# Kernel tuning notes

Measured on AMD Instinct MI355X. Metric: run time of the kernel, lower is better.

Reference implementation:

```python
import jax, jax.numpy as jnp
import numpy as np

LOG_2PI = float(np.log(2.0 * np.pi))


def setup_inputs() -> dict:
    key = jax.random.key(0)
    k1, k2, k3 = jax.random.split(key, 3)
    N, D, K = 2_000_000, 16, 32
    data = jax.random.normal(k1, (N, D), dtype=jnp.float32)
    means = jax.random.uniform(k2, (K, D), dtype=jnp.float32)  # torch.rand init
    # torch init is eye expanded per component; perturb slightly so the
    # Cholesky / solve paths are exercised with non-trivial values while
    # A @ A.T stays well-conditioned PD.
    cov_parts = (jnp.eye(D, dtype=jnp.float32)[None, :, :]
                 + 0.1 * jax.random.normal(k3, (K, D, D), dtype=jnp.float32))
    log_weights = jnp.zeros((K,), dtype=jnp.float32)
    return {"data": data, "means": means, "cov_parts": cov_parts,
            "log_weights": log_weights}


def _mixture_loglik(data, means, cov_parts, log_weights):
    D = data.shape[-1]
    # covariance_k = A_k @ A_k^T  -> Cholesky factor L_k (lower)
    cov = jnp.einsum('kij,klj->kil', cov_parts, cov_parts)      # [K, D, D]
    chol = jnp.linalg.cholesky(cov)                             # [K, D, D]

    def comp_logprob(mu, L):
        # MVN log_prob for one component over all N points
        diff = data - mu                                        # [N, D]
        # solve L z = diff^T  -> z: [D, N]
        z = jax.scipy.linalg.solve_triangular(L, diff.T, lower=True)
        quad = jnp.sum(z * z, axis=0)                           # [N]
        logdet = jnp.sum(jnp.log(jnp.diagonal(L)))              # 0.5*logdet(cov)
        return -0.5 * (quad + D * LOG_2PI) - logdet             # [N]

    # [N, K] log-likelihood per point per component
    log_liks = jax.vmap(comp_logprob, in_axes=(0, 0), out_axes=1)(means, chol)
    weighted = log_liks + log_weights ** 2                      # note: squared, per source
    return jnp.mean(jax.nn.logsumexp(weighted, axis=1))


def reference(data, means, cov_parts, log_weights):
    return _mixture_loglik(data, means, cov_parts, log_weights)
```

## Files before the change

### kernel.cpp

```cpp
#include <hip/hip_runtime.h>
#include <math.h>


#define LOG_2PI 1.8378770664093453f
#define INV_LN2 1.4426950408889634f
#define LN2_D   0.6931471805599453

typedef float    float4v __attribute__((ext_vector_type(4)));
typedef float    f32x16  __attribute__((ext_vector_type(16)));
typedef _Float16 f16x8   __attribute__((ext_vector_type(8)));
typedef _Float16 f16x2   __attribute__((ext_vector_type(2)));

union H8 { f16x8 h8; f16x2 h2[4]; };

#if __has_builtin(__builtin_amdgcn_exp2f)
#define EXP2F(x) __builtin_amdgcn_exp2f(x)
#else
#define EXP2F(x) exp2f(x)
#endif
#if __has_builtin(__builtin_amdgcn_logf)
#define LOG2F(x) __builtin_amdgcn_logf(x)
#else
#define LOG2F(x) log2f(x)
#endif

static __device__ __forceinline__ f16x2 pk2(float a, float b) {
#if __has_builtin(__builtin_amdgcn_cvt_pkrtz)
  return __builtin_bit_cast(f16x2, __builtin_amdgcn_cvt_pkrtz(a, b));
#else
  f16x2 r; r[0] = (_Float16)a; r[1] = (_Float16)b; return r;
#endif
}

static __device__ __forceinline__ float partner32(float x, bool lo) {
#if __has_builtin(__builtin_amdgcn_permlane32_swap)
  typedef unsigned u32x2 __attribute__((ext_vector_type(2)));
  unsigned u = __builtin_bit_cast(unsigned, x);
  u32x2 r = __builtin_amdgcn_permlane32_swap(u, u, false, false);
  return __builtin_bit_cast(float, lo ? r[1] : r[0]);
#else
  return __shfl_xor(x, 32, 64);
#endif
}

static __device__ __forceinline__ f16x2 sel2(bool c, f16x2 a, f16x2 b) {
  unsigned ua = __builtin_bit_cast(unsigned, a);
  unsigned ub = __builtin_bit_cast(unsigned, b);
  return __builtin_bit_cast(f16x2, c ? ua : ub);
}

__global__ void setup_kernel(const float* __restrict__ means,
                             const float* __restrict__ cov_parts,
                             const float* __restrict__ log_weights,
                             _Float16* __restrict__ W)
{
  const int k = blockIdx.x;
  const int i = threadIdx.x;

  __shared__ float sA[16][17];
  __shared__ float sC[16][17];
  __shared__ float sMu[16];
  __shared__ float sR[16];

  if (i < 16) {
    #pragma unroll
    for (int j = 0; j < 16; ++j) sA[i][j] = cov_parts[(k*16 + i)*16 + j];
    sMu[i] = means[k*16 + i];
  }
  __syncthreads();

  if (i < 16) {
    #pragma unroll
    for (int j = 0; j < 16; ++j) {
      float acc = 0.f;
      #pragma unroll
      for (int l = 0; l < 16; ++l) acc += sA[i][l] * sA[j][l];
      sC[i][j] = acc;
    }
  }
  __syncthreads();

  for (int j = 0; j < 16; ++j) {
    if (i == j) {
      float d = sC[j][j];
      for (int l = 0; l < j; ++l) d -= sC[j][l]*sC[j][l];
      sC[j][j] = sqrtf(d);
    }
    __syncthreads();
    if (i < 16 && i > j) {
      float a = sC[i][j];
      for (int l = 0; l < j; ++l) a -= sC[i][l]*sC[j][l];
      sC[i][j] = a / sC[j][j];
    }
    __syncthreads();
  }

  if (i < 16) {
    float y[16];
    #pragma unroll
    for (int r = 0; r < 16; ++r) {
      float a = (r == i) ? 1.f : 0.f;
      #pragma unroll
      for (int l = 0; l < r; ++l) a -= sC[r][l] * y[l];
      y[r] = a / sC[r][r];
    }
    #pragma unroll
    for (int r = 0; r < 16; ++r) sA[r][i] = y[r];
  }
  __syncthreads();

  if (i < 16) {
    float p[16];
    #pragma unroll
    for (int j = 0; j < 16; ++j) {
      float acc = 0.f;
      #pragma unroll
      for (int l = 0; l < 16; ++l) acc += sA[l][i] * sA[l][j];
      p[j] = acc;
    }
    float ri = 0.f;
    #pragma unroll
    for (int j = 0; j < 16; ++j) ri += p[j] * sMu[j];
    sR[i] = ri;

    #pragma unroll
    for (int j = 0; j < 16; ++j) {
      W[(size_t)(i*64 + (k + 32*(j >> 3)))*8 + (j & 7)] =
          (_Float16)(-0.5f * INV_LN2 * p[j]);
    }
    W[(size_t)(16*64 + (k + 32*(i >> 3)))*8 + (i & 7)] =
        (_Float16)(INV_LN2 * ri);
  }
  __syncthreads();

  if (i == 0) {
    float logdet = 0.f;
    #pragma unroll
    for (int j = 0; j < 16; ++j) logdet += __logf(sC[j][j]);
    float mupmu = 0.f;
    #pragma unroll
    for (int j = 0; j < 16; ++j) mupmu += sMu[j] * sR[j];
    float lw = log_weights[k];
    float c2v = INV_LN2 * (-0.5f*(mupmu + 16.f*LOG_2PI) - logdet + lw*lw);
    #pragma unroll
    for (int v = 0; v < 8; ++v) {
      W[(size_t)(17*64 + k)*8 + v]      = (v == 0) ? (_Float16)c2v : (_Float16)0.f;
      W[(size_t)(17*64 + k + 32)*8 + v] = (_Float16)0.f;
    }
  }
}

__global__ __launch_bounds__(256, 3) void main_kernel(
    const float* __restrict__ data,
    const _Float16* __restrict__ W,
    float* __restrict__ partials,
    int ntiles)
{
  const int lane = threadIdx.x & 63;
  const int n32  = lane & 31;
  const bool lo  = lane < 32;
  const int gwave  = (int)((blockIdx.x * blockDim.x + threadIdx.x) >> 6);
  const int nwaves = (int)((gridDim.x * blockDim.x) >> 6);

  f16x8 Wf[18];
  #pragma unroll
  for (int c = 0; c < 18; ++c)
    Wf[c] = *(const f16x8*)(W + (size_t)(c*64 + lane)*8);

  H8 bC;
  #pragma unroll
  for (int j = 0; j < 4; ++j) bC.h2[j] = pk2(0.f, 0.f);
  if (lo) bC.h2[0] = pk2(1.f, 0.f);

  float accsum = 0.f;

  const char* ptr = (const char*)data + ((size_t)gwave*2048 + (size_t)n32*64);
  const size_t step = (size_t)nwaves * 2048;

  float4v p0, p1, p2, p3;
  if (gwave < ntiles) {
    p0 = *(const float4v*)(ptr);      p1 = *(const float4v*)(ptr + 16);
    p2 = *(const float4v*)(ptr + 32); p3 = *(const float4v*)(ptr + 48);
  }

  for (int t = gwave; t < ntiles; t += nwaves) {
    f16x2 xh[8];
    xh[0] = pk2(p0[0], p0[1]); xh[1] = pk2(p0[2], p0[3]);
    xh[2] = pk2(p1[0], p1[1]); xh[3] = pk2(p1[2], p1[3]);
    xh[4] = pk2(p2[0], p2[1]); xh[5] = pk2(p2[2], p2[3]);
    xh[6] = pk2(p3[0], p3[1]); xh[7] = pk2(p3[2], p3[3]);

    ptr += step;
    if (t + nwaves < ntiles) {
      p0 = *(const float4v*)(ptr);      p1 = *(const float4v*)(ptr + 16);
      p2 = *(const float4v*)(ptr + 32); p3 = *(const float4v*)(ptr + 48);
    }

    f16x2 xs[4];
    #pragma unroll
    for (int j = 0; j < 4; ++j) xs[j] = sel2(lo, xh[j], xh[4+j]);

    f32x16 acc;
    #pragma unroll
    for (int r = 0; r < 16; ++r) acc[r] = 0.f;

    #pragma unroll
    for (int c = 0; c < 16; ++c) {
      _Float16 xi = xh[c >> 1][c & 1];
      H8 b;
      #pragma unroll
      for (int j = 0; j < 4; ++j) b.h2[j] = xs[j] * xi;
      acc = __builtin_amdgcn_mfma_f32_32x32x16_f16(Wf[c], b.h8, acc, 0, 0, 0);
    }
    {
      H8 b;
      #pragma unroll
      for (int j = 0; j < 4; ++j) b.h2[j] = xs[j];
      acc = __builtin_amdgcn_mfma_f32_32x32x16_f16(Wf[16], b.h8, acc, 0, 0, 0);
    }
    acc = __builtin_amdgcn_mfma_f32_32x32x16_f16(Wf[17], bC.h8, acc, 0, 0, 0);

    float m = acc[0];
    #pragma unroll
    for (int r = 1; r < 16; ++r) m = fmaxf(m, acc[r]);
    m = fmaxf(m, partner32(m, lo));
    float s = 0.f;
    #pragma unroll
    for (int r = 0; r < 16; ++r) s += EXP2F(acc[r] - m);
    s += partner32(s, lo);
    accsum += m + LOG2F(s);
  }

  #pragma unroll
  for (int off = 1; off <= 32; off <<= 1)
    accsum += __shfl_xor(accsum, off, 64);

  __shared__ float wsum[4];
  const int wid = (int)(threadIdx.x >> 6);
  if ((threadIdx.x & 63) == 0) wsum[wid] = accsum;
  __syncthreads();
  if (threadIdx.x == 0)
    partials[blockIdx.x] = wsum[0] + wsum[1] + wsum[2] + wsum[3];
}

__global__ void reduce_kernel(const float* __restrict__ partials, int n,
                              float* __restrict__ out, double scale)
{
  __shared__ double sd[256];
  double a = 0.0;
  for (int idx = threadIdx.x; idx < n; idx += 256) a += (double)partials[idx];
  sd[threadIdx.x] = a;
  __syncthreads();
  for (int s = 128; s > 0; s >>= 1) {
    if ((int)threadIdx.x < s) sd[threadIdx.x] += sd[threadIdx.x + s];
    __syncthreads();
  }
  if (threadIdx.x == 0) out[0] = (float)(sd[0] * scale);
}

extern "C" void kernel_launch(void* const* d_in, const int* in_sizes, int n_in,
                              void* d_out, int out_size, void* d_ws, size_t ws_size,
                              hipStream_t stream)
{
  const float* data        = (const float*)d_in[0];
  const float* means       = (const float*)d_in[1];
  const float* cov_parts   = (const float*)d_in[2];
  const float* log_weights = (const float*)d_in[3];

  const int npts   = in_sizes[0] / 16;
  const int ntiles = npts / 32;

  _Float16* W      = (_Float16*)d_ws;
  float*    partials = (float*)((char*)d_ws + (size_t)18*64*8*sizeof(_Float16));

  const int GRID = 768, BLOCK = 256;
  setup_kernel<<<32, 64, 0, stream>>>(means, cov_parts, log_weights, W);
  main_kernel<<<GRID, BLOCK, 0, stream>>>(data, W, partials, ntiles);
  reduce_kernel<<<1, 256, 0, stream>>>(partials, GRID, (float*)d_out,
                                       LN2_D / (2.0 * (double)npts));
}
```

Baseline: 202.8 us.

## Double-buffer data prefetch and fuse final reduction via last-block atomic counter

The main loop now keeps two tiles in flight, alternating between two register buffers so each load has a full iteration more latency cover. The separate reduce kernel is removed: each block publishes its partial, increments a global counter reset in the setup kernel, and the last block performs the double-precision reduction. This saves one kernel launch and adds prefetch depth, at the cost of extra registers under the occupancy-3 launch bound and an atomic plus fences per block.

```diff
diff --git a/kernel.cpp b/kernel.cpp
--- a/kernel.cpp
+++ b/kernel.cpp
@@ -52,10 +52,13 @@
 __global__ void setup_kernel(const float* __restrict__ means,
                              const float* __restrict__ cov_parts,
                              const float* __restrict__ log_weights,
-                             _Float16* __restrict__ W)
+                             _Float16* __restrict__ W,
+                             unsigned* __restrict__ counter)
 {
   const int k = blockIdx.x;
   const int i = threadIdx.x;
+
+  if (k == 0 && i == 0) counter[0] = 0u;
 
   __shared__ float sA[16][17];
   __shared__ float sC[16][17];
@@ -154,6 +157,9 @@
     const float* __restrict__ data,
     const _Float16* __restrict__ W,
     float* __restrict__ partials,
+    unsigned* __restrict__ counter,
+    float* __restrict__ out,
+    double scale,
     int ntiles)
 {
   const int lane = threadIdx.x & 63;
@@ -174,26 +180,32 @@
 
   float accsum = 0.f;
 
-  const char* ptr = (const char*)data + ((size_t)gwave*2048 + (size_t)n32*64);
-  const size_t step = (size_t)nwaves * 2048;
-
-  float4v p0, p1, p2, p3;
+  const char* ptrA = (const char*)data + ((size_t)gwave*2048 + (size_t)n32*64);
+  const char* ptrB = ptrA + (size_t)nwaves*2048;
+  const size_t step2 = (size_t)nwaves * 4096;
+
+  float4v pA0, pA1, pA2, pA3, pB0, pB1, pB2, pB3;
   if (gwave < ntiles) {
-    p0 = *(const float4v*)(ptr);      p1 = *(const float4v*)(ptr + 16);
-    p2 = *(const float4v*)(ptr + 32); p3 = *(const float4v*)(ptr + 48);
-  }
-
-  for (int t = gwave; t < ntiles; t += nwaves) {
+    pA0 = *(const float4v*)(ptrA);      pA1 = *(const float4v*)(ptrA + 16);
+    pA2 = *(const float4v*)(ptrA + 32); pA3 = *(const float4v*)(ptrA + 48);
+  }
+  if (gwave + nwaves < ntiles) {
+    pB0 = *(const float4v*)(ptrB);      pB1 = *(const float4v*)(ptrB + 16);
+    pB2 = *(const float4v*)(ptrB + 32); pB3 = *(const float4v*)(ptrB + 48);
+  }
+
+  auto body = [&](float4v& q0, float4v& q1, float4v& q2, float4v& q3,
+                  const char*& qptr, int t) {
     f16x2 xh[8];
-    xh[0] = pk2(p0[0], p0[1]); xh[1] = pk2(p0[2], p0[3]);
-    xh[2] = pk2(p1[0], p1[1]); xh[3] = pk2(p1[2], p1[3]);
-    xh[4] = pk2(p2[0], p2[1]); xh[5] = pk2(p2[2], p2[3]);
-    xh[6] = pk2(p3[0], p3[1]); xh[7] = pk2(p3[2], p3[3]);
-
-    ptr += step;
-    if (t + nwaves < ntiles) {
-      p0 = *(const float4v*)(ptr);      p1 = *(const float4v*)(ptr + 16);
-      p2 = *(const float4v*)(ptr + 32); p3 = *(const float4v*)(ptr + 48);
+    xh[0] = pk2(q0[0], q0[1]); xh[1] = pk2(q0[2], q0[3]);
+    xh[2] = pk2(q1[0], q1[1]); xh[3] = pk2(q1[2], q1[3]);
+    xh[4] = pk2(q2[0], q2[1]); xh[5] = pk2(q2[2], q2[3]);
+    xh[6] = pk2(q3[0], q3[1]); xh[7] = pk2(q3[2], q3[3]);
+
+    qptr += step2;
+    if (t + 2*nwaves < ntiles) {
+      q0 = *(const float4v*)(qptr);      q1 = *(const float4v*)(qptr + 16);
+      q2 = *(const float4v*)(qptr + 32); q3 = *(const float4v*)(qptr + 48);
     }
 
     f16x2 xs[4];
@@ -229,6 +241,16 @@
     for (int r = 0; r < 16; ++r) s += EXP2F(acc[r] - m);
     s += partner32(s, lo);
     accsum += m + LOG2F(s);
+  };
+
+  if (gwave < ntiles) {
+    int t = gwave;
+    for (;;) {
+      body(pA0, pA1, pA2, pA3, ptrA, t);
+      t += nwaves; if (t >= ntiles) break;
+      body(pB0, pB1, pB2, pB3, ptrB, t);
+      t += nwaves; if (t >= ntiles) break;
+    }
   }
 
   #pragma unroll
@@ -236,26 +258,32 @@
     accsum += __shfl_xor(accsum, off, 64);
 
   __shared__ float wsum[4];
+  __shared__ int isLast;
   const int wid = (int)(threadIdx.x >> 6);
   if ((threadIdx.x & 63) == 0) wsum[wid] = accsum;
   __syncthreads();
-  if (threadIdx.x == 0)
+  if (threadIdx.x == 0) {
     partials[blockIdx.x] = wsum[0] + wsum[1] + wsum[2] + wsum[3];
-}
-
-__global__ void reduce_kernel(const float* __restrict__ partials, int n,
-                              float* __restrict__ out, double scale)
-{
-  __shared__ double sd[256];
-  double a = 0.0;
-  for (int idx = threadIdx.x; idx < n; idx += 256) a += (double)partials[idx];
-  sd[threadIdx.x] = a;
-  __syncthreads();
-  for (int s = 128; s > 0; s >>= 1) {
-    if ((int)threadIdx.x < s) sd[threadIdx.x] += sd[threadIdx.x + s];
+    __threadfence();
+    unsigned old = atomicAdd(counter, 1u);
+    isLast = (old == gridDim.x - 1) ? 1 : 0;
+  }
+  __syncthreads();
+
+  if (isLast) {
+    __threadfence();
+    __shared__ double sd[256];
+    double a = 0.0;
+    for (int idx = (int)threadIdx.x; idx < (int)gridDim.x; idx += 256)
+      a += (double)partials[idx];
+    sd[threadIdx.x] = a;
     __syncthreads();
-  }
-  if (threadIdx.x == 0) out[0] = (float)(sd[0] * scale);
+    for (int s = 128; s > 0; s >>= 1) {
+      if ((int)threadIdx.x < s) sd[threadIdx.x] += sd[threadIdx.x + s];
+      __syncthreads();
+    }
+    if (threadIdx.x == 0) out[0] = (float)(sd[0] * scale);
+  }
 }
 
 extern "C" void kernel_launch(void* const* d_in, const int* in_sizes, int n_in,
@@ -270,12 +298,13 @@
   const int npts   = in_sizes[0] / 16;
   const int ntiles = npts / 32;
 
-  _Float16* W      = (_Float16*)d_ws;
-  float*    partials = (float*)((char*)d_ws + (size_t)18*64*8*sizeof(_Float16));
+  _Float16* W        = (_Float16*)d_ws;
+  float*    partials = (float*)((char*)d_ws + 18432);
+  unsigned* counter  = (unsigned*)((char*)d_ws + 18432 + 3072);
 
   const int GRID = 768, BLOCK = 256;
-  setup_kernel<<<32, 64, 0, stream>>>(means, cov_parts, log_weights, W);
-  main_kernel<<<GRID, BLOCK, 0, stream>>>(data, W, partials, ntiles);
-  reduce_kernel<<<1, 256, 0, stream>>>(partials, GRID, (float*)d_out,
-                                       LN2_D / (2.0 * (double)npts));
-}
+  setup_kernel<<<32, 64, 0, stream>>>(means, cov_parts, log_weights, W, counter);
+  main_kernel<<<GRID, BLOCK, 0, stream>>>(data, W, partials, counter,
+                                          (float*)d_out,
+                                          LN2_D / (2.0 * (double)npts), ntiles);
+}
```

After: 234.4 us. +15.5%, slower.

## Fuse final reduction into main kernel via last-block atomic and raise occupancy

Applied to the files above, without the earlier changes.

Replaces the separate reduce kernel with a last-block-done pattern: each block writes its partial, increments an atomic counter, and the final block performs the double-precision reduction. The counter is reset in the setup kernel. Launch bounds go from 3 to 4 blocks per SM and the grid from 768 to 2048 blocks, and the max/exp-sum reductions are rewritten as trees for more ILP. This removes one kernel launch and adds an atomic plus threadfence per block, and the tighter register budget may cause spills.

```diff
diff --git a/kernel.cpp b/kernel.cpp
--- a/kernel.cpp
+++ b/kernel.cpp
@@ -52,10 +52,13 @@
 __global__ void setup_kernel(const float* __restrict__ means,
                              const float* __restrict__ cov_parts,
                              const float* __restrict__ log_weights,
-                             _Float16* __restrict__ W)
+                             _Float16* __restrict__ W,
+                             unsigned* __restrict__ counter)
 {
   const int k = blockIdx.x;
   const int i = threadIdx.x;
+
+  if (k == 0 && i == 0) counter[0] = 0u;
 
   __shared__ float sA[16][17];
   __shared__ float sC[16][17];
@@ -150,16 +153,20 @@
   }
 }
 
-__global__ __launch_bounds__(256, 3) void main_kernel(
+__global__ __launch_bounds__(256, 4) void main_kernel(
     const float* __restrict__ data,
     const _Float16* __restrict__ W,
     float* __restrict__ partials,
+    unsigned* __restrict__ counter,
+    float* __restrict__ out,
+    double scale,
     int ntiles)
 {
-  const int lane = threadIdx.x & 63;
+  const int tid  = (int)threadIdx.x;
+  const int lane = tid & 63;
   const int n32  = lane & 31;
   const bool lo  = lane < 32;
-  const int gwave  = (int)((blockIdx.x * blockDim.x + threadIdx.x) >> 6);
+  const int gwave  = (int)((blockIdx.x * blockDim.x + tid) >> 6);
   const int nwaves = (int)((gridDim.x * blockDim.x) >> 6);
 
   f16x8 Wf[18];
@@ -220,13 +227,33 @@
     }
     acc = __builtin_amdgcn_mfma_f32_32x32x16_f16(Wf[17], bC.h8, acc, 0, 0, 0);
 
-    float m = acc[0];
-    #pragma unroll
-    for (int r = 1; r < 16; ++r) m = fmaxf(m, acc[r]);
+    float mx0 = fmaxf(acc[0],  acc[8]);
+    float mx1 = fmaxf(acc[1],  acc[9]);
+    float mx2 = fmaxf(acc[2],  acc[10]);
+    float mx3 = fmaxf(acc[3],  acc[11]);
+    float mx4 = fmaxf(acc[4],  acc[12]);
+    float mx5 = fmaxf(acc[5],  acc[13]);
+    float mx6 = fmaxf(acc[6],  acc[14]);
+    float mx7 = fmaxf(acc[7],  acc[15]);
+    mx0 = fmaxf(mx0, mx4); mx1 = fmaxf(mx1, mx5);
+    mx2 = fmaxf(mx2, mx6); mx3 = fmaxf(mx3, mx7);
+    mx0 = fmaxf(mx0, mx2); mx1 = fmaxf(mx1, mx3);
+    float m = fmaxf(mx0, mx1);
     m = fmaxf(m, partner32(m, lo));
-    float s = 0.f;
-    #pragma unroll
-    for (int r = 0; r < 16; ++r) s += EXP2F(acc[r] - m);
+
+    float e0  = EXP2F(acc[0]  - m), e1  = EXP2F(acc[1]  - m);
+    float e2  = EXP2F(acc[2]  - m), e3  = EXP2F(acc[3]  - m);
+    float e4  = EXP2F(acc[4]  - m), e5  = EXP2F(acc[5]  - m);
+    float e6  = EXP2F(acc[6]  - m), e7  = EXP2F(acc[7]  - m);
+    float e8  = EXP2F(acc[8]  - m), e9  = EXP2F(acc[9]  - m);
+    float e10 = EXP2F(acc[10] - m), e11 = EXP2F(acc[11] - m);
+    float e12 = EXP2F(acc[12] - m), e13 = EXP2F(acc[13] - m);
+    float e14 = EXP2F(acc[14] - m), e15 = EXP2F(acc[15] - m);
+    e0 += e8;  e1 += e9;  e2 += e10; e3 += e11;
+    e4 += e12; e5 += e13; e6 += e14; e7 += e15;
+    e0 += e4;  e1 += e5;  e2 += e6;  e3 += e7;
+    e0 += e2;  e1 += e3;
+    float s = e0 + e1;
     s += partner32(s, lo);
     accsum += m + LOG2F(s);
   }
@@ -236,26 +263,32 @@
     accsum += __shfl_xor(accsum, off, 64);
 
   __shared__ float wsum[4];
-  const int wid = (int)(threadIdx.x >> 6);
-  if ((threadIdx.x & 63) == 0) wsum[wid] = accsum;
-  __syncthreads();
-  if (threadIdx.x == 0)
+  __shared__ int isLast;
+  const int wid = tid >> 6;
+  if ((tid & 63) == 0) wsum[wid] = accsum;
+  __syncthreads();
+  if (tid == 0) {
     partials[blockIdx.x] = wsum[0] + wsum[1] + wsum[2] + wsum[3];
-}
-
-__global__ void reduce_kernel(const float* __restrict__ partials, int n,
-                              float* __restrict__ out, double scale)
-{
-  __shared__ double sd[256];
-  double a = 0.0;
-  for (int idx = threadIdx.x; idx < n; idx += 256) a += (double)partials[idx];
-  sd[threadIdx.x] = a;
-  __syncthreads();
-  for (int s = 128; s > 0; s >>= 1) {
-    if ((int)threadIdx.x < s) sd[threadIdx.x] += sd[threadIdx.x + s];
+    __threadfence();
+    unsigned old = atomicAdd(counter, 1u);
+    isLast = (old == gridDim.x - 1) ? 1 : 0;
+  }
+  __syncthreads();
+
+  if (isLast) {
+    __threadfence();
+    __shared__ double sd[256];
+    double a = 0.0;
+    for (int idx = tid; idx < (int)gridDim.x; idx += 256)
+      a += (double)partials[idx];
+    sd[tid] = a;
     __syncthreads();
-  }
-  if (threadIdx.x == 0) out[0] = (float)(sd[0] * scale);
+    for (int s2 = 128; s2 > 0; s2 >>= 1) {
+      if (tid < s2) sd[tid] += sd[tid + s2];
+      __syncthreads();
+    }
+    if (tid == 0) out[0] = (float)(sd[0] * scale);
+  }
 }
 
 extern "C" void kernel_launch(void* const* d_in, const int* in_sizes, int n_in,
@@ -270,12 +303,13 @@
   const int npts   = in_sizes[0] / 16;
   const int ntiles = npts / 32;
 
-  _Float16* W      = (_Float16*)d_ws;
-  float*    partials = (float*)((char*)d_ws + (size_t)18*64*8*sizeof(_Float16));
-
-  const int GRID = 768, BLOCK = 256;
-  setup_kernel<<<32, 64, 0, stream>>>(means, cov_parts, log_weights, W);
-  main_kernel<<<GRID, BLOCK, 0, stream>>>(data, W, partials, ntiles);
-  reduce_kernel<<<1, 256, 0, stream>>>(partials, GRID, (float*)d_out,
-                                       LN2_D / (2.0 * (double)npts));
-}
+  _Float16* W        = (_Float16*)d_ws;
+  float*    partials = (float*)((char*)d_ws + 18432);
+  unsigned* counter  = (unsigned*)((char*)d_ws + 18432 + 8192);
+
+  const int GRID = 2048, BLOCK = 256;
+  setup_kernel<<<32, 64, 0, stream>>>(means, cov_parts, log_weights, W, counter);
+  main_kernel<<<GRID, BLOCK, 0, stream>>>(data, W, partials, counter,
+                                          (float*)d_out,
+                                          LN2_D / (2.0 * (double)npts), ntiles);
+}
```

Result: slower. 298.9 us (+47.4%).
